# Kernel optimization log

Measured on AMD Instinct MI355X. Metric: run time of the kernel, lower is better.

Reference implementation:

```python
import jax, jax.numpy as jnp
import numpy as np

K = 2            # kernel_size
NQ = K * K       # 4 qubits
DEPTH = 1


def _apply1(state, U, q):
    # state: (N,2,2,2,2) complex; apply 2x2 gate U on qubit q
    s = jnp.moveaxis(state, 1 + q, -1)
    s = s @ U.T
    return jnp.moveaxis(s, -1, 1 + q)


def _cnot(state, c, t):
    s = jnp.moveaxis(state, (1 + c, 1 + t), (-2, -1))  # (...,2c,2t)
    s = jnp.stack([s[..., 0, :], s[..., 1, ::-1]], axis=-2)
    return jnp.moveaxis(s, (-2, -1), (1 + c, 1 + t))


def _rx(w):
    c, s = jnp.cos(w / 2), jnp.sin(w / 2)
    return jnp.array([[1, 0], [0, 1]], jnp.complex64) * c + jnp.array([[0, -1j], [-1j, 0]], jnp.complex64) * s


def _ry(w):
    c, s = jnp.cos(w / 2), jnp.sin(w / 2)
    return jnp.array([[1, 0], [0, 1]], jnp.complex64) * c + jnp.array([[0, -1], [1, 0]], jnp.complex64) * s


def setup_inputs() -> dict:
    key = jax.random.key(0)
    k1, k2, k3 = jax.random.split(key, 3)
    B, C, H = 1024, 1, 28
    F = H - K + 1
    n_feat = NQ * C * F * F  # 2916
    x = jax.random.uniform(k1, (B, C, H, H), dtype=jnp.float32)
    W = jax.random.normal(k2, (10, n_feat), dtype=jnp.float32)
    b = jax.random.normal(k3, (10,), dtype=jnp.float32)
    weights = jnp.zeros((DEPTH, NQ), dtype=jnp.float32)  # forward() uses zeros, not the Parameter
    return {"x": x, "W": W, "b": b, "weights": weights}


def reference(x, W, b, weights):
    B, C, H, _ = x.shape
    F = H - K + 1
    # extract all KxK patches, row-major within the patch (matches img[c,i:i+k,j:j+k].reshape(-1))
    p = jnp.stack([x[:, :, i:i + F, j:j + F] for i in range(K) for j in range(K)], axis=-1)  # (B,C,F,F,4)
    ang = p.reshape(-1, NQ) * jnp.pi  # AngleEmbedding angles, (N,4)
    # product state from per-qubit RY(theta)|0> = [cos(t/2), sin(t/2)]
    a = jnp.stack([jnp.cos(ang / 2), jnp.sin(ang / 2)], axis=-1).astype(jnp.complex64)  # (N,4,2)
    state = jnp.einsum('na,nb,nc,nd->nabcd', a[:, 0], a[:, 1], a[:, 2], a[:, 3])
    for l in range(DEPTH):
        w = weights[l]
        state = _apply1(state, _rx(w[0]), 0)
        state = _apply1(state, _rx(w[1]), 1)
        state = _cnot(state, 2, 3)
        state = _cnot(state, 0, 2)
        state = _cnot(state, 0, 3)
        state = _apply1(state, _ry(w[2]), 0)
        state = _apply1(state, _ry(w[3]), 3)
    probs = state.real ** 2 + state.imag ** 2  # (N,2,2,2,2)
    z = jnp.array([1.0, -1.0], dtype=x.dtype)
    evs = []
    for q in range(NQ):
        axes = tuple(ax for ax in range(1, 5) if ax != 1 + q)
        evs.append(probs.sum(axes) @ z)  # <Z_q>, (N,)
    evs = jnp.stack(evs, axis=-1)  # (N, 4)
    # per-image reorder: (C*F*F, 4) -> transpose -> (4*C, F, F)
    q = evs.reshape(B, C, F, F, NQ)
    q = jnp.transpose(q, (0, 4, 1, 2, 3)).reshape(B, NQ * C * F * F)
    return q @ W.T + b
```

## Files before the change

kernel.cpp:

```cpp
#include <hip/hip_runtime.h>


#define HD 28
#define FD 27
#define NPATCH (FD * FD)
#define NOUT 10

__global__ __launch_bounds__(256)
void hqnn_fused(const float* __restrict__ x,
                const float* __restrict__ W,
                const float* __restrict__ bias,
                const float* __restrict__ wts,
                float* __restrict__ out)
{
    __shared__ float sc[HD * HD];
    __shared__ float ss[HD * HD];
    __shared__ float red[4][NOUT];

    const int b   = blockIdx.x;
    const int tid = threadIdx.x;

    const float w0 = wts[0], w1 = wts[1], w2 = wts[2], w3 = wts[3];
    const float cw0 = cosf(w0);
    const float cw1 = cosf(w1);
    const float cw2 = cosf(w2), sw2 = sinf(w2);
    const float cw3 = cosf(w3), sw3 = sinf(w3);

    const float* xb = x + b * (HD * HD);
    for (int i = tid; i < HD * HD; i += 256) {
        float s, c;
        sincospif(xb[i], &s, &c);
        sc[i] = c;
        ss[i] = s;
    }
    __syncthreads();

    float acc[NOUT];
#pragma unroll
    for (int o = 0; o < NOUT; ++o) acc[o] = 0.f;

    for (int idx = tid; idx < NPATCH; idx += 256) {
        const int fi = idx / FD;
        const int fj = idx - fi * FD;
        const int p  = fi * HD + fj;

        const float c00 = sc[p];
        const float c01 = sc[p + 1];
        const float c10 = sc[p + HD];
        const float c11 = sc[p + HD + 1];
        const float s00 = ss[p];
        const float s10 = ss[p + HD];
        const float s11 = ss[p + HD + 1];

        const float ev0 = cw2 * cw0 * c00 - sw2 * s00 * s10;
        const float ev1 = cw1 * c01;
        const float ev2 = cw0 * c00 * c10;
        const float ev3 = cw3 * ev2 * c11 - sw3 * s11;

        const float* Wp = W + idx;
#pragma unroll
        for (int o = 0; o < NOUT; ++o) {
            const float* Wo = Wp + o * (4 * NPATCH);
            acc[o] += ev0 * Wo[0]
                    + ev1 * Wo[NPATCH]
                    + ev2 * Wo[2 * NPATCH]
                    + ev3 * Wo[3 * NPATCH];
        }
    }

#pragma unroll
    for (int o = 0; o < NOUT; ++o) {
#pragma unroll
        for (int off = 32; off >= 1; off >>= 1)
            acc[o] += __shfl_down(acc[o], off, 64);
    }
    const int lane = tid & 63;
    const int wv   = tid >> 6;
    if (lane == 0) {
#pragma unroll
        for (int o = 0; o < NOUT; ++o) red[wv][o] = acc[o];
    }
    __syncthreads();
    if (tid < NOUT) {
        out[b * NOUT + tid] =
            red[0][tid] + red[1][tid] + red[2][tid] + red[3][tid] + bias[tid];
    }
}

extern "C" void kernel_launch(void* const* d_in, const int* in_sizes, int n_in,
                              void* d_out, int out_size, void* d_ws, size_t ws_size,
                              hipStream_t stream) {
    const float* x    = (const float*)d_in[0];
    const float* W    = (const float*)d_in[1];
    const float* bias = (const float*)d_in[2];
    const float* wts  = (const float*)d_in[3];
    float* out = (float*)d_out;

    const int B = in_sizes[0] / (HD * HD);
    hqnn_fused<<<B, 256, 0, stream>>>(x, W, bias, wts, out);
}
```

Baseline: 68.35 us.

## Stage per-patch expectations in LDS and vectorize W dot products with float4

Each block now writes all 2916 expectation values to shared memory, then runs a separate pass that reads W and the features as float4 vectors, one group of four contiguous features per thread. The input image is also loaded as float4, and the wave-shuffle reduction is replaced by a padded shared-memory partial-sum reduction. The goal is wider, coalesced global loads of W, at the cost of extra LDS traffic, an additional barrier and more shared memory per block.

```diff
diff --git a/kernel.cpp b/kernel.cpp
--- a/kernel.cpp
+++ b/kernel.cpp
@@ -3,8 +3,11 @@
 
 #define HD 28
 #define FD 27
-#define NPATCH (FD * FD)
+#define NPATCH 729
+#define NF 2916
+#define NG (NF / 4)
 #define NOUT 10
+#define PSTR 257
 
 __global__ __launch_bounds__(256)
 void hqnn_fused(const float* __restrict__ x,
@@ -15,7 +18,8 @@
 {
     __shared__ float sc[HD * HD];
     __shared__ float ss[HD * HD];
-    __shared__ float red[4][NOUT];
+    __shared__ __align__(16) float evl[NF];
+    __shared__ float part[NOUT * PSTR];
 
     const int b   = blockIdx.x;
     const int tid = threadIdx.x;
@@ -26,22 +30,23 @@
     const float cw2 = cosf(w2), sw2 = sinf(w2);
     const float cw3 = cosf(w3), sw3 = sinf(w3);
 
-    const float* xb = x + b * (HD * HD);
-    for (int i = tid; i < HD * HD; i += 256) {
-        float s, c;
-        sincospif(xb[i], &s, &c);
-        sc[i] = c;
-        ss[i] = s;
+    const float4* xb4 = (const float4*)(x + b * (HD * HD));
+    if (tid < 196) {
+        const float4 v = xb4[tid];
+        float s0, c0, s1, c1, s2, c2, s3, c3;
+        sincospif(v.x, &s0, &c0);
+        sincospif(v.y, &s1, &c1);
+        sincospif(v.z, &s2, &c2);
+        sincospif(v.w, &s3, &c3);
+        const int p4 = tid * 4;
+        sc[p4] = c0; sc[p4 + 1] = c1; sc[p4 + 2] = c2; sc[p4 + 3] = c3;
+        ss[p4] = s0; ss[p4 + 1] = s1; ss[p4 + 2] = s2; ss[p4 + 3] = s3;
     }
     __syncthreads();
 
-    float acc[NOUT];
-#pragma unroll
-    for (int o = 0; o < NOUT; ++o) acc[o] = 0.f;
-
-    for (int idx = tid; idx < NPATCH; idx += 256) {
-        const int fi = idx / FD;
-        const int fj = idx - fi * FD;
+    for (int pp = tid; pp < NPATCH; pp += 256) {
+        const int fi = pp / FD;
+        const int fj = pp - fi * FD;
         const int p  = fi * HD + fj;
 
         const float c00 = sc[p];
@@ -52,38 +57,44 @@
         const float s10 = ss[p + HD];
         const float s11 = ss[p + HD + 1];
 
-        const float ev0 = cw2 * cw0 * c00 - sw2 * s00 * s10;
-        const float ev1 = cw1 * c01;
         const float ev2 = cw0 * c00 * c10;
-        const float ev3 = cw3 * ev2 * c11 - sw3 * s11;
+        evl[pp]               = cw2 * cw0 * c00 - sw2 * s00 * s10;
+        evl[NPATCH + pp]      = cw1 * c01;
+        evl[2 * NPATCH + pp]  = ev2;
+        evl[3 * NPATCH + pp]  = cw3 * ev2 * c11 - sw3 * s11;
+    }
+    __syncthreads();
 
-        const float* Wp = W + idx;
+    float acc[NOUT];
+#pragma unroll
+    for (int o = 0; o < NOUT; ++o) acc[o] = 0.f;
+
+    const float4* W4  = (const float4*)W;
+    const float4* ev4 = (const float4*)evl;
+    for (int g = tid; g < NG; g += 256) {
+        const float4 e = ev4[g];
 #pragma unroll
         for (int o = 0; o < NOUT; ++o) {
-            const float* Wo = Wp + o * (4 * NPATCH);
-            acc[o] += ev0 * Wo[0]
-                    + ev1 * Wo[NPATCH]
-                    + ev2 * Wo[2 * NPATCH]
-                    + ev3 * Wo[3 * NPATCH];
+            const float4 w = W4[o * NG + g];
+            acc[o] += e.x * w.x + e.y * w.y + e.z * w.z + e.w * w.w;
         }
     }
 
 #pragma unroll
-    for (int o = 0; o < NOUT; ++o) {
+    for (int o = 0; o < NOUT; ++o) part[o * PSTR + tid] = acc[o];
+    __syncthreads();
+
+    if (tid < NOUT * 16) {
+        const int o = tid >> 4;
+        const int j = tid & 15;
+        float s = 0.f;
 #pragma unroll
-        for (int off = 32; off >= 1; off >>= 1)
-            acc[o] += __shfl_down(acc[o], off, 64);
-    }
-    const int lane = tid & 63;
-    const int wv   = tid >> 6;
-    if (lane == 0) {
-#pragma unroll
-        for (int o = 0; o < NOUT; ++o) red[wv][o] = acc[o];
-    }
-    __syncthreads();
-    if (tid < NOUT) {
-        out[b * NOUT + tid] =
-            red[0][tid] + red[1][tid] + red[2][tid] + red[3][tid] + bias[tid];
+        for (int k = 0; k < 256; k += 16) s += part[o * PSTR + j + k];
+        s += __shfl_down(s, 8, 16);
+        s += __shfl_down(s, 4, 16);
+        s += __shfl_down(s, 2, 16);
+        s += __shfl_down(s, 1, 16);
+        if (j == 0) out[b * NOUT + o] = s + bias[o];
     }
 }
 
```

New measurement: 66.75 us. -2.3%, faster.
